# Kernel tuning notes

Hardware: AMD Instinct MI355X
Metric: run time of the kernel (lower is better)

## Reference

```python
import jax, jax.numpy as jnp
import numpy as np

MIN_V, MAX_V, NORM = 0.0, 4.0, 4.0
NUM_HEADS = 8
BN_EPS = 1e-5

@jax.custom_vjp
def quant(x):
    return jnp.round(jnp.clip(x, MIN_V, MAX_V))

def _quant_fwd(x):
    return jnp.round(jnp.clip(x, MIN_V, MAX_V)), x

def _quant_bwd(x, g):
    # straight-through: zero grad outside [min, max]
    return (jnp.where((x < MIN_V) | (x > MAX_V), 0.0, g),)

quant.defvjp(_quant_fwd, _quant_bwd)

def spike(x):
    return quant(x) / NORM

def conv_bn(x, w, gamma, beta, mean, var):
    # 1x1 conv (no bias) + BatchNorm2d (eval mode, running stats)
    y = jnp.einsum('oc,bchw->bohw', w, x)
    s = gamma / jnp.sqrt(var + BN_EPS)
    return y * s[None, :, None, None] + (beta - mean * s)[None, :, None, None]


def setup_inputs() -> dict:
    key = jax.random.key(0)
    B, C, H, W = 8, 384, 64, 64
    ks = jax.random.split(key, 21)
    d = {'x': jax.random.normal(ks[0], (B, C, H, W), jnp.float32)}
    i = 1
    for p in ('q', 'k', 'v', 'p'):
        d[f'{p}_w'] = jax.random.normal(ks[i], (C, C), jnp.float32) * 0.05; i += 1
        d[f'{p}_gamma'] = jax.random.uniform(ks[i], (C,), jnp.float32, 0.5, 1.5); i += 1
        d[f'{p}_beta'] = jax.random.normal(ks[i], (C,), jnp.float32) * 0.1; i += 1
        d[f'{p}_mean'] = jax.random.normal(ks[i], (C,), jnp.float32) * 0.1; i += 1
        d[f'{p}_var'] = jax.random.uniform(ks[i], (C,), jnp.float32, 0.5, 1.5); i += 1
    return d


def reference(x, q_w, q_gamma, q_beta, q_mean, q_var,
              k_w, k_gamma, k_beta, k_mean, k_var,
              v_w, v_gamma, v_beta, v_mean, v_var,
              p_w, p_gamma, p_beta, p_mean, p_var):
    B, C, H, W = x.shape
    N = H * W
    hd = C // NUM_HEADS
    scale = hd ** -0.5

    xs = spike(x)
    q = spike(conv_bn(xs, q_w, q_gamma, q_beta, q_mean, q_var))
    k = spike(conv_bn(xs, k_w, k_gamma, k_beta, k_mean, k_var))
    v = spike(conv_bn(xs, v_w, v_gamma, v_beta, v_mean, v_var))

    # (B,C,H,W) -> (B,heads,N,hd); channel c = h*hd + d
    def to_heads(t):
        return t.reshape(B, NUM_HEADS, hd, N).transpose(0, 1, 3, 2)

    q, k, v = to_heads(q), to_heads(k), to_heads(v)

    # softmax-free attention: (q @ k^T) @ v == q @ (k^T @ v)  -> O(N*d^2)
    kv = jnp.einsum('bhnd,bhne->bhde', k, v)          # [B,H,hd,hd]
    attn = jnp.einsum('bhnd,bhde->bhne', q, kv) * (scale * 2)  # [B,H,N,hd]

    # back to (B, C_v, N): torch does transpose(2,3).reshape(B,C_v,N)
    a = attn.transpose(0, 1, 3, 2).reshape(B, C, N)
    a = spike(a).reshape(B, C, H, W)
    out = conv_bn(a, p_w, p_gamma, p_beta, p_mean, p_var)
    return out
```

## Files before the change

kernel.cpp:

```cpp
#include <hip/hip_runtime.h>
#include <stdint.h>

#define B_  8
#define C_  384
#define N_  4096
#define NH_ 8
#define HD_ 48
#define CB_ (C_*N_)
#define KS2 768

typedef __attribute__((ext_vector_type(8))) short short8;
typedef __attribute__((ext_vector_type(8))) _Float16 half8;
typedef __attribute__((ext_vector_type(4))) float f32x4;

struct P5 { const float *w, *g, *be, *mu, *va; };
struct W4 { const float *w0, *w1, *w2, *w3; };

__device__ __forceinline__ float b2f(unsigned short u) {
    union { unsigned int i; float f; } c; c.i = ((unsigned int)u) << 16; return c.f;
}
__device__ __forceinline__ unsigned short f2b(float f) {
    union { float f; unsigned int i; } c; c.f = f;
    return (unsigned short)((c.i + 0x7FFFu + ((c.i >> 16) & 1u)) >> 16);
}
__device__ __forceinline__ unsigned short f2h(float f) {
    union { _Float16 h; unsigned short u; } c; c.h = (_Float16)f; return c.u;
}
__device__ __forceinline__ float spikef(float f) {
    f = fminf(fmaxf(f, 0.0f), 4.0f);
    return rintf(f) * 0.25f;
}
__device__ __forceinline__ void async16(const void* g, void* l) {
    __builtin_amdgcn_global_load_lds((const __attribute__((address_space(1))) void*)g,
                                     (__attribute__((address_space(3))) void*)l, 16, 0, 0);
}

__global__ __launch_bounds__(256) void k_prep(W4 ws4, unsigned short* __restrict__ wsp) {
    int idx = blockIdx.x * 256 + threadIdx.x;
    if (idx >= 589824) return;
    int mat = idx / 147456, rem = idx % 147456;
    int o = rem / 384, c = rem % 384;
    const float* W = (mat == 0) ? ws4.w0 : (mat == 1) ? ws4.w1 : (mat == 2) ? ws4.w2 : ws4.w3;
    float w = W[o * 384 + c];
    _Float16 hh = (fabsf(w) < 6.103515625e-05f) ? (_Float16)0 : (_Float16)w;
    float r1 = w - (float)hh;
    float s  = r1 * 4096.0f;
    union { _Float16 h; unsigned short u; } ch, cl;
    ch.h = hh; cl.h = (_Float16)s;
    unsigned short* row = wsp + (size_t)mat * 384 * KS2 + (size_t)o * KS2 + c;
    row[0] = cl.u; row[384] = ch.u;
}

__global__ __launch_bounds__(256) void k0_spike_T(const float* __restrict__ x,
                                                  unsigned short* __restrict__ xst) {
    int nt = blockIdx.x, ct = blockIdx.y, b = blockIdx.z;
    int t = threadIdx.x;
    __shared__ __attribute__((aligned(16))) unsigned short sm[64][68];
    int n0 = nt * 64, c0 = ct * 64;
    const float* xb = x + (size_t)b * CB_;
    #pragma unroll
    for (int i = 0; i < 4; ++i) {
        int c = (t >> 4) + 16 * i;
        int seg = t & 15;
        float4 d = *(const float4*)(xb + (size_t)(c0 + c) * N_ + n0 + seg * 4);
        unsigned short v[4];
        v[0] = f2h(spikef(d.x)); v[1] = f2h(spikef(d.y));
        v[2] = f2h(spikef(d.z)); v[3] = f2h(spikef(d.w));
        *(uint2*)&sm[c][seg * 4] = *(const uint2*)v;
    }
    __syncthreads();
    unsigned short* ob = xst + (size_t)b * CB_;
    #pragma unroll
    for (int i = 0; i < 2; ++i) {
        int flat = i * 256 + t;
        int n = flat >> 3, segc = flat & 7;
        unsigned short v[8];
        #pragma unroll
        for (int j = 0; j < 8; ++j) v[j] = sm[segc * 8 + j][n];
        *(uint4*)(ob + (size_t)(n0 + n) * C_ + c0 + segc * 8) = *(const uint4*)v;
    }
}

__global__ __launch_bounds__(256) void k1_qkv(const unsigned short* __restrict__ xst,
                                              const unsigned short* __restrict__ wsp,
                                              P5 pq, P5 pk, P5 pv,
                                              unsigned short* __restrict__ qs,
                                              unsigned short* __restrict__ ks,
                                              unsigned short* __restrict__ vs) {
    int gid = blockIdx.x;
    int xcd = gid & 7, idx = gid >> 3;
    int pairSlot = idx / 9, mt = idx - pairSlot * 9;
    int p = xcd * 32 + pairSlot;
    int ntile = p >> 3, b = p & 7;
    int mat = mt / 3;
    int orow0 = (mt % 3) * 128;
    int n0 = ntile * 128;
    int t = threadIdx.x, lane = t & 63, wvv = t >> 6;
    int wr = wvv >> 1, wc = wvv & 1;

    __shared__ __attribute__((aligned(16))) short lds[17408];
    P5 pp = (mat == 0) ? pq : (mat == 1 ? pk : pv);
    const unsigned short* abase = xst + (size_t)b * CB_;
    const unsigned short* wbase = wsp + (size_t)mat * 384 * KS2;

    f32x4 acc[4][4] = {};
    for (int kk = 0; kk < KS2; kk += 64) {
        if (kk == 384) {
            #pragma unroll
            for (int mi = 0; mi < 4; ++mi)
                #pragma unroll
                for (int ni = 0; ni < 4; ++ni)
                    acc[mi][ni] = acc[mi][ni] * 0.000244140625f;
        }
        int ck = (kk >= 384) ? kk - 384 : kk;
        #pragma unroll
        for (int j = 0; j < 4; ++j) {
            int row = wvv * 32 + j * 8 + (lane >> 3);
            int g = (lane & 7) ^ (row & 7);
            async16(abase + (size_t)(n0 + row) * C_ + ck + g * 8, lds + (wvv * 32 + j * 8) * 64);
        }
        #pragma unroll
        for (int j = 0; j < 4; ++j) {
            int row = wvv * 32 + j * 8 + (lane >> 3);
            int g = (lane & 7) ^ (row & 7);
            async16(wbase + (size_t)(orow0 + row) * KS2 + kk + g * 8, lds + 8192 + (wvv * 32 + j * 8) * 64);
        }
        __syncthreads();
        #pragma unroll
        for (int ksb = 0; ksb < 2; ++ksb) {
            half8 af[4], bfr[4];
            #pragma unroll
            for (int mi = 0; mi < 4; ++mi) {
                int row = wr * 64 + mi * 16 + (lane & 15);
                int s = (ksb * 4 + (lane >> 4)) ^ (row & 7);
                af[mi] = *(const half8*)&lds[row * 64 + s * 8];
            }
            #pragma unroll
            for (int ni = 0; ni < 4; ++ni) {
                int row = wc * 64 + ni * 16 + (lane & 15);
                int s = (ksb * 4 + (lane >> 4)) ^ (row & 7);
                bfr[ni] = *(const half8*)&lds[8192 + row * 64 + s * 8];
            }
            #pragma unroll
            for (int mi = 0; mi < 4; ++mi)
                #pragma unroll
                for (int ni = 0; ni < 4; ++ni)
                    acc[mi][ni] = __builtin_amdgcn_mfma_f32_16x16x32_f16(af[mi], bfr[ni], acc[mi][ni], 0, 0, 0);
        }
        __syncthreads();
    }

    float s_bn[4], t_bn[4];
    #pragma unroll
    for (int ni = 0; ni < 4; ++ni) {
        int o = orow0 + wc * 64 + ni * 16 + (lane & 15);
        float g = pp.g[o], be = pp.be[o], mu = pp.mu[o], va = pp.va[o];
        float s = g / sqrtf(va + 1e-5f);
        s_bn[ni] = s; t_bn[ni] = be - mu * s;
    }
    unsigned short* esm = (unsigned short*)lds;

    if (mat != 0) {
        #pragma unroll
        for (int mi = 0; mi < 4; ++mi)
            #pragma unroll
            for (int ni = 0; ni < 4; ++ni) {
                int ol = wc * 64 + ni * 16 + (lane & 15);
                int nb = wr * 64 + mi * 16 + (lane >> 4) * 4;
                unsigned short vv[4];
                #pragma unroll
                for (int r = 0; r < 4; ++r)
                    vv[r] = f2b(spikef(acc[mi][ni][r] * s_bn[ni] + t_bn[ni]));
                *(uint2*)&esm[ol * 136 + nb] = *(const uint2*)vv;
            }
        __syncthreads();
        unsigned short* dst = ((mat == 1) ? ks : vs) + (size_t)b * CB_;
        #pragma unroll
        for (int i = 0; i < 8; ++i) {
            int o = (t >> 4) + 16 * i;
            int seg = t & 15;
            uint4 d = *(const uint4*)&esm[o * 136 + seg * 8];
            *(uint4*)(dst + (size_t)(orow0 + o) * N_ + n0 + seg * 8) = d;
        }
    } else {
        #pragma unroll
        for (int mi = 0; mi < 4; ++mi)
            #pragma unroll
            for (int ni = 0; ni < 4; ++ni) {
                int ol = wc * 64 + ni * 16 + (lane & 15);
                int nb = wr * 64 + mi * 16 + (lane >> 4) * 4;
                #pragma unroll
                for (int r = 0; r < 4; ++r)
                    esm[(nb + r) * 136 + ol] = f2b(spikef(acc[mi][ni][r] * s_bn[ni] + t_bn[ni]));
            }
        __syncthreads();
        #pragma unroll
        for (int i = 0; i < 8; ++i) {
            int n = (t >> 4) + 16 * i;
            int seg = t & 15;
            uint4 d = *(const uint4*)&esm[n * 136 + seg * 8];
            *(uint4*)(qs + ((size_t)b * N_ + n0 + n) * C_ + orow0 + seg * 8) = d;
        }
    }
}

__global__ __launch_bounds__(256) void k2_kv(const unsigned short* __restrict__ ks,
                                             const unsigned short* __restrict__ vs,
                                             float* __restrict__ kvf) {
    int id = blockIdx.x;
    int b = id >> 7, h = (id >> 4) & 7, ck = id & 15;
    int t = threadIdx.x, lane = t & 63, w = t >> 6;
    const unsigned short* kb = ks + (size_t)b * CB_ + h * HD_ * N_;
    const unsigned short* vb = vs + (size_t)b * CB_ + h * HD_ * N_;
    int kbase = ck * 256 + w * 64;

    f32x4 acc[3][3] = {};
    #pragma unroll
    for (int kk = 0; kk < 64; kk += 32) {
        int n = kbase + kk + (lane >> 4) * 8;
        short8 af[3], bfr[3];
        #pragma unroll
        for (int di = 0; di < 3; ++di)
            af[di] = *(const short8*)(kb + (size_t)((lane & 15) + 16 * di) * N_ + n);
        #pragma unroll
        for (int ei = 0; ei < 3; ++ei)
            bfr[ei] = *(const short8*)(vb + (size_t)((lane & 15) + 16 * ei) * N_ + n);
        #pragma unroll
        for (int di = 0; di < 3; ++di)
            #pragma unroll
            for (int ei = 0; ei < 3; ++ei)
                acc[di][ei] = __builtin_amdgcn_mfma_f32_16x16x32_bf16(af[di], bfr[ei], acc[di][ei], 0, 0, 0);
    }
    __shared__ float red[4][48][48];
    #pragma unroll
    for (int di = 0; di < 3; ++di)
        #pragma unroll
        for (int ei = 0; ei < 3; ++ei) {
            int d0 = di * 16 + (lane >> 4) * 4;
            int e = ei * 16 + (lane & 15);
            #pragma unroll
            for (int r = 0; r < 4; ++r) red[w][d0 + r][e] = acc[di][ei][r];
        }
    __syncthreads();
    for (int i = t; i < 2304; i += 256) {
        int e = i / 48, d = i % 48;
        float sum = red[0][d][e] + red[1][d][e] + red[2][d][e] + red[3][d][e];
        atomicAdd(&kvf[(b * NH_ + h) * 2304 + e * 48 + d], sum);
    }
}

__global__ __launch_bounds__(256) void k2b_split(const float* __restrict__ kvf,
                                                 unsigned short* __restrict__ hi,
                                                 unsigned short* __restrict__ lo) {
    int i = blockIdx.x * 256 + threadIdx.x;
    if (i >= 64 * 48 * 64) return;
    int d = i & 63; int rest = i >> 6;
    unsigned short h16 = 0, l16 = 0;
    if (d < 48) {
        float v = kvf[rest * 48 + d];
        h16 = f2b(v);
        l16 = f2b(v - b2f(h16));
    }
    hi[i] = h16; lo[i] = l16;
}

__global__ __launch_bounds__(256) void k3_attn(const unsigned short* __restrict__ qs,
                                               const unsigned short* __restrict__ hi,
                                               const unsigned short* __restrict__ lo,
                                               unsigned short* __restrict__ as_) {
    int id = blockIdx.x;
    int b = id >> 6, nt = id & 63;
    int t = threadIdx.x, lane = t & 63, w = t >> 6;
    int nb0 = nt * 64;
    int n0 = nb0 + w * 16;
    const unsigned short* qb = qs + ((size_t)b * N_ + n0) * C_;
    const float S2 = 0.28867513459481287f;
    __shared__ __attribute__((aligned(16))) unsigned short sm[64][392];

    for (int h = 0; h < NH_; ++h) {
        f32x4 acc[3] = {};
        #pragma unroll
        for (int ksb = 0; ksb < 2; ++ksb) {
            int koff = h * HD_ + ksb * 32 + (lane >> 4) * 8;
            short8 a = *(const short8*)(qb + (size_t)(lane & 15) * C_ + koff);
            #pragma unroll
            for (int ei = 0; ei < 3; ++ei) {
                int e = ei * 16 + (lane & 15);
                size_t boff = ((size_t)(b * NH_ + h) * HD_ + e) * 64 + ksb * 32 + (lane >> 4) * 8;
                short8 bh = *(const short8*)(hi + boff);
                short8 bl = *(const short8*)(lo + boff);
                acc[ei] = __builtin_amdgcn_mfma_f32_16x16x32_bf16(a, bh, acc[ei], 0, 0, 0);
                acc[ei] = __builtin_amdgcn_mfma_f32_16x16x32_bf16(a, bl, acc[ei], 0, 0, 0);
            }
        }
        #pragma unroll
        for (int ei = 0; ei < 3; ++ei) {
            int e = ei * 16 + (lane & 15);
            #pragma unroll
            for (int r = 0; r < 4; ++r)
                sm[w * 16 + (lane >> 4) * 4 + r][h * HD_ + e] = f2h(spikef(acc[ei][r] * S2));
        }
    }
    __syncthreads();
    unsigned short* ob = as_ + ((size_t)b * N_ + nb0) * C_;
    #pragma unroll
    for (int i = 0; i < 12; ++i) {
        int f = i * 256 + t;
        int row = f / 48, seg = f % 48;
        uint4 d = *(const uint4*)&sm[row][seg * 8];
        *(uint4*)(ob + (size_t)row * C_ + seg * 8) = d;
    }
}

__global__ __launch_bounds__(256) void k4_pconv(const unsigned short* __restrict__ as_,
                                                const unsigned short* __restrict__ wsp,
                                                P5 pp,
                                                float* __restrict__ out) {
    int gid = blockIdx.x;
    int xcd = gid & 7, idx = gid >> 3;
    int pairSlot = idx / 3, mt = idx - pairSlot * 3;
    int p = xcd * 32 + pairSlot;
    int ntile = p >> 3, b = p & 7;
    int orow0 = mt * 128;
    int n0 = ntile * 128;
    int t = threadIdx.x, lane = t & 63, wvv = t >> 6;
    int wr = wvv >> 1, wc = wvv & 1;

    __shared__ __attribute__((aligned(16))) short lds[16384];
    const unsigned short* abase = as_ + (size_t)b * CB_;
    const unsigned short* wbase = wsp + (size_t)3 * 384 * KS2;

    f32x4 acc[4][4] = {};
    for (int kk = 0; kk < KS2; kk += 64) {
        if (kk == 384) {
            #pragma unroll
            for (int mi = 0; mi < 4; ++mi)
                #pragma unroll
                for (int ni = 0; ni < 4; ++ni)
                    acc[mi][ni] = acc[mi][ni] * 0.000244140625f;
        }
        int ck = (kk >= 384) ? kk - 384 : kk;
        #pragma unroll
        for (int j = 0; j < 4; ++j) {
            int row = wvv * 32 + j * 8 + (lane >> 3);
            int g = (lane & 7) ^ (row & 7);
            async16(abase + (size_t)(n0 + row) * C_ + ck + g * 8, lds + (wvv * 32 + j * 8) * 64);
        }
        #pragma unroll
        for (int j = 0; j < 4; ++j) {
            int row = wvv * 32 + j * 8 + (lane >> 3);
            int g = (lane & 7) ^ (row & 7);
            async16(wbase + (size_t)(orow0 + row) * KS2 + kk + g * 8, lds + 8192 + (wvv * 32 + j * 8) * 64);
        }
        __syncthreads();
        #pragma unroll
        for (int ksb = 0; ksb < 2; ++ksb) {
            half8 af[4], bfr[4];
            #pragma unroll
            for (int mi = 0; mi < 4; ++mi) {
                int row = wr * 64 + mi * 16 + (lane & 15);
                int s = (ksb * 4 + (lane >> 4)) ^ (row & 7);
                af[mi] = *(const half8*)&lds[row * 64 + s * 8];
            }
            #pragma unroll
            for (int ni = 0; ni < 4; ++ni) {
                int row = wc * 64 + ni * 16 + (lane & 15);
                int s = (ksb * 4 + (lane >> 4)) ^ (row & 7);
                bfr[ni] = *(const half8*)&lds[8192 + row * 64 + s * 8];
            }
            #pragma unroll
            for (int mi = 0; mi < 4; ++mi)
                #pragma unroll
                for (int ni = 0; ni < 4; ++ni)
                    acc[mi][ni] = __builtin_amdgcn_mfma_f32_16x16x32_f16(af[mi], bfr[ni], acc[mi][ni], 0, 0, 0);
        }
        __syncthreads();
    }

    float s_bn[4], t_bn[4];
    #pragma unroll
    for (int ni = 0; ni < 4; ++ni) {
        int o = orow0 + wc * 64 + ni * 16 + (lane & 15);
        float g = pp.g[o], be = pp.be[o], mu = pp.mu[o], va = pp.va[o];
        float s = g / sqrtf(va + 1e-5f);
        s_bn[ni] = s; t_bn[ni] = be - mu * s;
    }
    #pragma unroll
    for (int mi = 0; mi < 4; ++mi)
        #pragma unroll
        for (int ni = 0; ni < 4; ++ni) {
            int o = orow0 + wc * 64 + ni * 16 + (lane & 15);
            int n = n0 + wr * 64 + mi * 16 + (lane >> 4) * 4;
            f32x4 vv;
            #pragma unroll
            for (int r = 0; r < 4; ++r)
                vv[r] = acc[mi][ni][r] * s_bn[ni] + t_bn[ni];
            *(f32x4*)(out + ((size_t)b * C_ + o) * N_ + n) = vv;
        }
}

extern "C" void kernel_launch(void* const* d_in, const int* in_sizes, int n_in,
                              void* d_out, int out_size, void* d_ws, size_t ws_size,
                              hipStream_t stream) {
    P5 pq { (const float*)d_in[1],  (const float*)d_in[2],  (const float*)d_in[3],
            (const float*)d_in[4],  (const float*)d_in[5] };
    P5 pk { (const float*)d_in[6],  (const float*)d_in[7],  (const float*)d_in[8],
            (const float*)d_in[9],  (const float*)d_in[10] };
    P5 pv { (const float*)d_in[11], (const float*)d_in[12], (const float*)d_in[13],
            (const float*)d_in[14], (const float*)d_in[15] };
    P5 pp { (const float*)d_in[16], (const float*)d_in[17], (const float*)d_in[18],
            (const float*)d_in[19], (const float*)d_in[20] };
    W4 w4 { pq.w, pk.w, pv.w, pp.w };

    char* ws = (char*)d_ws;
    const size_t S = (size_t)B_ * C_ * N_ * 2;
    unsigned short* xst = (unsigned short*)ws;
    unsigned short* qs  = (unsigned short*)(ws + S);
    unsigned short* ks  = (unsigned short*)(ws + 2 * S + 256);
    unsigned short* vs  = (unsigned short*)(ws + 3 * S + 512);
    float*          kvf = (float*)(ws + 4 * S + 768);
    unsigned short* hi  = (unsigned short*)(ws + 4 * S + 768 + 589824);
    unsigned short* lo  = (unsigned short*)(ws + 4 * S + 768 + 589824 + 393216);
    unsigned short* wsp = (unsigned short*)(ws + 4 * S + 768 + 589824 + 2 * 393216);
    unsigned short* as_ = xst;

    hipMemsetAsync(kvf, 0, 589824, stream);
    k_prep<<<2304, 256, 0, stream>>>(w4, wsp);
    k0_spike_T<<<dim3(64, 6, 8), 256, 0, stream>>>((const float*)d_in[0], xst);
    k1_qkv<<<2304, 256, 0, stream>>>(xst, wsp, pq, pk, pv, qs, ks, vs);
    k2_kv<<<1024, 256, 0, stream>>>(ks, vs, kvf);
    k2b_split<<<768, 256, 0, stream>>>(kvf, hi, lo);
    k3_attn<<<512, 256, 0, stream>>>(qs, hi, lo, as_);
    k4_pconv<<<768, 256, 0, stream>>>(as_, wsp, pp, (float*)d_out);
}
```

Baseline: 272.0 us.

## Fuse kv split into attention kernel, fold memset into prep, stage pconv output

The memset of the kv accumulator moves into the weight-prep kernel, and the separate hi/lo bf16 split kernel is folded into the attention kernel. The attention kernel now splits per-head kv into LDS itself and async-loads q tiles into swizzled LDS. It is also split across two head groups to double the grid. The projection conv epilogue stages results through LDS so the fp32 output is written in coalesced rows along N. This removes two launches and some global traffic, at the cost of redundant kv splitting per block and extra LDS and barriers.

Result: no change. 268.4 us (-1.3%).

```diff
diff --git a/kernel.cpp b/kernel.cpp
--- a/kernel.cpp
+++ b/kernel.cpp
@@ -35,9 +35,11 @@
                                      (__attribute__((address_space(3))) void*)l, 16, 0, 0);
 }
 
-__global__ __launch_bounds__(256) void k_prep(W4 ws4, unsigned short* __restrict__ wsp) {
+__global__ __launch_bounds__(256) void k_prep(W4 ws4, unsigned short* __restrict__ wsp,
+                                              float* __restrict__ kvf) {
     int idx = blockIdx.x * 256 + threadIdx.x;
     if (idx >= 589824) return;
+    if (idx < 147456) kvf[idx] = 0.0f;
     int mat = idx / 147456, rem = idx % 147456;
     int o = rem / 384, c = rem % 384;
     const float* W = (mat == 0) ? ws4.w0 : (mat == 1) ? ws4.w1 : (mat == 2) ? ws4.w2 : ws4.w3;
@@ -249,66 +251,83 @@
     }
 }
 
-__global__ __launch_bounds__(256) void k2b_split(const float* __restrict__ kvf,
-                                                 unsigned short* __restrict__ hi,
-                                                 unsigned short* __restrict__ lo) {
-    int i = blockIdx.x * 256 + threadIdx.x;
-    if (i >= 64 * 48 * 64) return;
-    int d = i & 63; int rest = i >> 6;
-    unsigned short h16 = 0, l16 = 0;
-    if (d < 48) {
-        float v = kvf[rest * 48 + d];
-        h16 = f2b(v);
-        l16 = f2b(v - b2f(h16));
-    }
-    hi[i] = h16; lo[i] = l16;
-}
-
 __global__ __launch_bounds__(256) void k3_attn(const unsigned short* __restrict__ qs,
-                                               const unsigned short* __restrict__ hi,
-                                               const unsigned short* __restrict__ lo,
+                                               const float* __restrict__ kvf,
                                                unsigned short* __restrict__ as_) {
     int id = blockIdx.x;
-    int b = id >> 6, nt = id & 63;
+    int hg = id & 1, nt = (id >> 1) & 63, b = id >> 7;
     int t = threadIdx.x, lane = t & 63, w = t >> 6;
     int nb0 = nt * 64;
-    int n0 = nb0 + w * 16;
-    const unsigned short* qb = qs + ((size_t)b * N_ + n0) * C_;
+    __shared__ __attribute__((aligned(16))) unsigned short ldsq[64 * 24 * 8];
+    __shared__ __attribute__((aligned(16))) unsigned short ldsh[48 * 72];
+    __shared__ __attribute__((aligned(16))) unsigned short ldsl[48 * 72];
+
+    const unsigned short* qb = qs + ((size_t)b * N_ + nb0) * C_ + hg * 192;
+    #pragma unroll
+    for (int i = 0; i < 6; ++i) {
+        int g = (i * 4 + w) * 64;
+        int f = g + lane;
+        int row = f / 24, sc = f % 24;
+        int c = sc ^ (row & 7);
+        async16(qb + (size_t)row * C_ + c * 8, ldsq + (size_t)g * 8);
+    }
+    const float* kvb = kvf + ((size_t)(b * NH_ + hg * 4)) * 2304;
     const float S2 = 0.28867513459481287f;
-    __shared__ __attribute__((aligned(16))) unsigned short sm[64][392];
-
-    for (int h = 0; h < NH_; ++h) {
+    int quad = lane >> 4;
+    int qrow = w * 16 + (lane & 15);
+
+    for (int hl = 0; hl < 4; ++hl) {
+        __syncthreads();
+        const float* kvh = kvb + hl * 2304;
+        for (int i = t; i < 48 * 64; i += 256) {
+            int e = i >> 6, d = i & 63;
+            unsigned short h16 = 0, l16 = 0;
+            if (d < 48) {
+                float v = kvh[e * 48 + d];
+                h16 = f2b(v);
+                l16 = f2b(v - b2f(h16));
+            }
+            ldsh[e * 72 + d] = h16;
+            ldsl[e * 72 + d] = l16;
+        }
+        __syncthreads();
+
         f32x4 acc[3] = {};
         #pragma unroll
         for (int ksb = 0; ksb < 2; ++ksb) {
-            int koff = h * HD_ + ksb * 32 + (lane >> 4) * 8;
-            short8 a = *(const short8*)(qb + (size_t)(lane & 15) * C_ + koff);
+            int c = hl * 6 + ksb * 4 + quad;
+            int cc = c > 23 ? 23 : c;
+            int slot = cc ^ (qrow & 7);
+            short8 a = *(const short8*)&ldsq[(qrow * 24 + slot) * 8];
             #pragma unroll
             for (int ei = 0; ei < 3; ++ei) {
                 int e = ei * 16 + (lane & 15);
-                size_t boff = ((size_t)(b * NH_ + h) * HD_ + e) * 64 + ksb * 32 + (lane >> 4) * 8;
-                short8 bh = *(const short8*)(hi + boff);
-                short8 bl = *(const short8*)(lo + boff);
+                short8 bh = *(const short8*)&ldsh[e * 72 + ksb * 32 + quad * 8];
+                short8 bl = *(const short8*)&ldsl[e * 72 + ksb * 32 + quad * 8];
                 acc[ei] = __builtin_amdgcn_mfma_f32_16x16x32_bf16(a, bh, acc[ei], 0, 0, 0);
                 acc[ei] = __builtin_amdgcn_mfma_f32_16x16x32_bf16(a, bl, acc[ei], 0, 0, 0);
             }
         }
         #pragma unroll
         for (int ei = 0; ei < 3; ++ei) {
-            int e = ei * 16 + (lane & 15);
-            #pragma unroll
-            for (int r = 0; r < 4; ++r)
-                sm[w * 16 + (lane >> 4) * 4 + r][h * HD_ + e] = f2h(spikef(acc[ei][r] * S2));
+            int col = hl * 48 + ei * 16 + (lane & 15);
+            int ch = col >> 3, j = col & 7;
+            #pragma unroll
+            for (int r = 0; r < 4; ++r) {
+                int row = w * 16 + quad * 4 + r;
+                ldsq[(row * 24 + (ch ^ (row & 7))) * 8 + j] = f2h(spikef(acc[ei][r] * S2));
+            }
         }
     }
     __syncthreads();
-    unsigned short* ob = as_ + ((size_t)b * N_ + nb0) * C_;
-    #pragma unroll
-    for (int i = 0; i < 12; ++i) {
+    unsigned short* ob = as_ + ((size_t)b * N_ + nb0) * C_ + hg * 192;
+    #pragma unroll
+    for (int i = 0; i < 6; ++i) {
         int f = i * 256 + t;
-        int row = f / 48, seg = f % 48;
-        uint4 d = *(const uint4*)&sm[row][seg * 8];
-        *(uint4*)(ob + (size_t)row * C_ + seg * 8) = d;
+        int row = f / 24, sc = f % 24;
+        int slot = sc ^ (row & 7);
+        uint4 d = *(const uint4*)&ldsq[(row * 24 + slot) * 8];
+        *(uint4*)(ob + (size_t)row * C_ + sc * 8) = d;
     }
 }
 
@@ -326,7 +345,8 @@
     int t = threadIdx.x, lane = t & 63, wvv = t >> 6;
     int wr = wvv >> 1, wc = wvv & 1;
 
-    __shared__ __attribute__((aligned(16))) short lds[16384];
+    __shared__ __attribute__((aligned(16))) char ldsb[33792];
+    short* lds = (short*)ldsb;
     const unsigned short* abase = as_ + (size_t)b * CB_;
     const unsigned short* wbase = wsp + (size_t)3 * 384 * KS2;
 
@@ -385,18 +405,32 @@
         float s = g / sqrtf(va + 1e-5f);
         s_bn[ni] = s; t_bn[ni] = be - mu * s;
     }
-    #pragma unroll
-    for (int mi = 0; mi < 4; ++mi)
-        #pragma unroll
-        for (int ni = 0; ni < 4; ++ni) {
-            int o = orow0 + wc * 64 + ni * 16 + (lane & 15);
-            int n = n0 + wr * 64 + mi * 16 + (lane >> 4) * 4;
-            f32x4 vv;
-            #pragma unroll
-            for (int r = 0; r < 4; ++r)
-                vv[r] = acc[mi][ni][r] * s_bn[ni] + t_bn[ni];
-            *(f32x4*)(out + ((size_t)b * C_ + o) * N_ + n) = vv;
-        }
+    float* fsm = (float*)ldsb;
+    for (int half = 0; half < 2; ++half) {
+        __syncthreads();
+        if (wc == half) {
+            #pragma unroll
+            for (int mi = 0; mi < 4; ++mi)
+                #pragma unroll
+                for (int ni = 0; ni < 4; ++ni) {
+                    int ol = ni * 16 + (lane & 15);
+                    int nl = wr * 64 + mi * 16 + (lane >> 4) * 4;
+                    f32x4 vv;
+                    #pragma unroll
+                    for (int r = 0; r < 4; ++r)
+                        vv[r] = acc[mi][ni][r] * s_bn[ni] + t_bn[ni];
+                    *(f32x4*)&fsm[ol * 132 + nl] = vv;
+                }
+        }
+        __syncthreads();
+        #pragma unroll
+        for (int i = 0; i < 8; ++i) {
+            int f = i * 256 + t;
+            int o = f >> 5, slot = f & 31;
+            f32x4 vv = *(const f32x4*)&fsm[o * 132 + slot * 4];
+            *(f32x4*)(out + ((size_t)b * C_ + orow0 + half * 64 + o) * N_ + n0 + slot * 4) = vv;
+        }
+    }
 }
 
 extern "C" void kernel_launch(void* const* d_in, const int* in_sizes, int n_in,
@@ -419,17 +453,13 @@
     unsigned short* ks  = (unsigned short*)(ws + 2 * S + 256);
     unsigned short* vs  = (unsigned short*)(ws + 3 * S + 512);
     float*          kvf = (float*)(ws + 4 * S + 768);
-    unsigned short* hi  = (unsigned short*)(ws + 4 * S + 768 + 589824);
-    unsigned short* lo  = (unsigned short*)(ws + 4 * S + 768 + 589824 + 393216);
-    unsigned short* wsp = (unsigned short*)(ws + 4 * S + 768 + 589824 + 2 * 393216);
+    unsigned short* wsp = (unsigned short*)(ws + 4 * S + 768 + 589824);
     unsigned short* as_ = xst;
 
-    hipMemsetAsync(kvf, 0, 589824, stream);
-    k_prep<<<2304, 256, 0, stream>>>(w4, wsp);
+    k_prep<<<2304, 256, 0, stream>>>(w4, wsp, kvf);
     k0_spike_T<<<dim3(64, 6, 8), 256, 0, stream>>>((const float*)d_in[0], xst);
     k1_qkv<<<2304, 256, 0, stream>>>(xst, wsp, pq, pk, pv, qs, ks, vs);
     k2_kv<<<1024, 256, 0, stream>>>(ks, vs, kvf);
-    k2b_split<<<768, 256, 0, stream>>>(kvf, hi, lo);
-    k3_attn<<<512, 256, 0, stream>>>(qs, hi, lo, as_);
+    k3_attn<<<1024, 256, 0, stream>>>(qs, kvf, as_);
     k4_pconv<<<768, 256, 0, stream>>>(as_, wsp, pp, (float*)d_out);
 }
```
